# Performance work log

Hardware: AMD Instinct MI355X
Metric: run time of the kernel (lower is better)

The kernel has to match this reference:

```python
import jax, jax.numpy as jnp
import numpy as np

N_NODES = 50000
N_EDGES = 600000
N_FEAT = 128
HIDDEN = 128
OUT_CH = 128
N_GRAPHS = 64
BN_EPS = 1e-5


def gcn_conv(x, src, dst, ew, W, b):
    """PyG GCNConv: add self-loops, symmetric deg^{-1/2} normalization with edge weights."""
    n = x.shape[0]
    h = x @ W  # [N, out]
    loop = jnp.arange(n)
    src2 = jnp.concatenate([src, loop])
    dst2 = jnp.concatenate([dst, loop])
    w2 = jnp.concatenate([ew, jnp.ones((n,), x.dtype)])
    deg = jax.ops.segment_sum(w2, dst2, num_segments=n)
    dinv = jnp.where(deg > 0, jax.lax.rsqrt(deg), 0.0)
    norm = dinv[src2] * w2 * dinv[dst2]  # [E+N]
    out = jax.ops.segment_sum(h[src2] * norm[:, None], dst2, num_segments=n)
    return out + b


def setup_inputs() -> dict:
    key = jax.random.key(0)
    ks = jax.random.split(key, 12)
    x = jax.random.normal(ks[0], (N_NODES, N_FEAT), jnp.float32)
    edge_index = jax.random.randint(ks[1], (2, N_EDGES), 0, N_NODES, dtype=jnp.int64)
    batch = jnp.sort(jax.random.randint(ks[2], (N_NODES,), 0, N_GRAPHS, dtype=jnp.int64))
    edge_attr = jax.random.uniform(ks[3], (N_EDGES,), jnp.float32)
    s1 = 1.0 / np.sqrt(N_FEAT)
    s2 = 1.0 / np.sqrt(HIDDEN)
    s3 = 1.0 / np.sqrt(OUT_CH)
    s4 = 1.0 / np.sqrt(OUT_CH // 2)
    return {
        "x": x, "edge_index": edge_index, "batch": batch, "edge_attr": edge_attr,
        "W1": jax.random.uniform(ks[4], (N_FEAT, HIDDEN), jnp.float32, -s1, s1),
        "b1": jnp.zeros((HIDDEN,), jnp.float32),
        "W2": jax.random.uniform(ks[5], (HIDDEN, OUT_CH), jnp.float32, -s2, s2),
        "b2": jnp.zeros((OUT_CH,), jnp.float32),
        "fc1_W": jax.random.uniform(ks[6], (OUT_CH, OUT_CH // 2), jnp.float32, -s3, s3),
        "fc1_b": jax.random.uniform(ks[7], (OUT_CH // 2,), jnp.float32, -s3, s3),
        "bn_gamma": jnp.ones((OUT_CH // 2,), jnp.float32),
        "bn_beta": jnp.zeros((OUT_CH // 2,), jnp.float32),
        "fc3_W": jax.random.uniform(ks[8], (OUT_CH // 2, 1), jnp.float32, -s4, s4),
        "fc3_b": jax.random.uniform(ks[9], (1,), jnp.float32, -s4, s4),
    }


def reference(x, edge_index, batch, edge_attr, W1, b1, W2, b2,
              fc1_W, fc1_b, bn_gamma, bn_beta, fc3_W, fc3_b):
    src, dst = edge_index[0], edge_index[1]
    h = jax.nn.relu(gcn_conv(x, src, dst, edge_attr, W1, b1))
    # dropout skipped (deterministic eval: mode=False)
    h = jax.nn.relu(gcn_conv(h, src, dst, edge_attr, W2, b2))
    # global_mean_pool over batch segment ids
    sums = jax.ops.segment_sum(h, batch, num_segments=N_GRAPHS)  # [G, out]
    cnt = jax.ops.segment_sum(jnp.ones_like(batch, jnp.float32), batch, num_segments=N_GRAPHS)
    g = sums / jnp.maximum(cnt, 1.0)[:, None]
    z = jax.nn.relu(g @ fc1_W + fc1_b)
    # BatchNorm1d with batch statistics (training-mode math, biased var)
    mean = jnp.mean(z, axis=0)
    var = jnp.mean((z - mean) ** 2, axis=0)
    z = bn_gamma * (z - mean) * jax.lax.rsqrt(var + BN_EPS) + bn_beta
    return z @ fc3_W + fc3_b  # [G, 1]
```

## Files before the change

### kernel.cpp

```cpp
#include <hip/hip_runtime.h>

#define NNODES 50000
#define NEDGES 600000
#define NGRAPHS 64
#define BN_EPS 1e-5f
#define NB1 ((NNODES + 255) / 256)
#define PPG 16
#define GEMM_BLOCKS ((NNODES + 127) / 128)
#define NOWN 8
#define RANGE 6250
#define SEG 16
#define SEGI4 (NEDGES / SEG / 4)
#define HIST_BLOCKS (NOWN * SEG)


__device__ __forceinline__ void gemm_tile(const float* __restrict__ A,
        const float* __restrict__ W, float* __restrict__ C, int block) {
    __shared__ float a_lds[16][132];
    __shared__ float w_lds[16][192];
    const int tid = threadIdx.x;
    const int row0 = block * 128;
    const int tx = tid & 15;
    const int ty = tid >> 4;
    float acc[4][8];
#pragma unroll
    for (int i = 0; i < 4; ++i)
#pragma unroll
        for (int j = 0; j < 8; ++j) acc[i][j] = 0.f;

    for (int kc = 0; kc < 128; kc += 16) {
        {
            int r = tid >> 2;
            int k4 = (tid & 3) << 2;
            int grow = row0 + r;
            float4 v = make_float4(0.f, 0.f, 0.f, 0.f);
            if (grow < NNODES) v = *(const float4*)(A + (size_t)grow * 128 + kc + k4);
            a_lds[k4 + 0][r] = v.x; a_lds[k4 + 1][r] = v.y;
            a_lds[k4 + 2][r] = v.z; a_lds[k4 + 3][r] = v.w;
        }
        {
            int kk = tid >> 5;
            int c4 = tid & 31;
            float4 v = *(const float4*)(W + (size_t)(kc + kk) * 128 + c4 * 4);
            int sw = 12 * (c4 >> 1) + ((c4 & 1) << 2);
            *(float4*)&w_lds[kk][sw] = v;
        }
        __syncthreads();
#pragma unroll
        for (int k = 0; k < 16; ++k) {
            float a[4], b[8];
            *(float4*)&a[0] = *(const float4*)&a_lds[k][ty * 4];
            *(float4*)&b[0] = *(const float4*)&w_lds[k][tx * 12];
            *(float4*)&b[4] = *(const float4*)&w_lds[k][tx * 12 + 4];
#pragma unroll
            for (int i = 0; i < 4; ++i)
#pragma unroll
                for (int j = 0; j < 8; ++j)
                    acc[i][j] = fmaf(a[i], b[j], acc[i][j]);
        }
        __syncthreads();
    }
#pragma unroll
    for (int i = 0; i < 4; ++i) {
        int grow = row0 + ty * 4 + i;
        if (grow < NNODES) {
            float4 v0 = make_float4(acc[i][0], acc[i][1], acc[i][2], acc[i][3]);
            float4 v1 = make_float4(acc[i][4], acc[i][5], acc[i][6], acc[i][7]);
            *(float4*)(C + (size_t)grow * 128 + tx * 8) = v0;
            *(float4*)(C + (size_t)grow * 128 + tx * 8 + 4) = v1;
        }
    }
}

__global__ __launch_bounds__(512) void k_gemm1_hist(const float* __restrict__ A,
        const float* __restrict__ W, float* __restrict__ C,
        const int* __restrict__ dst, int* __restrict__ cnt_seg) {
    if (blockIdx.x >= GEMM_BLOCKS) {
        __shared__ int lh[RANGE];
        int t = threadIdx.x;
        int hb = blockIdx.x - GEMM_BLOCKS;
        int own = hb & (NOWN - 1);
        int seg = hb >> 3;
        int lo = own * RANGE;
        for (int i = t; i < RANGE; i += 512) lh[i] = 0;
        __syncthreads();
        const int4* d4 = (const int4*)dst;
        int q1 = (seg + 1) * SEGI4;
        for (int q = seg * SEGI4 + t; q < q1; q += 512) {
            int4 v = d4[q];
            unsigned a0 = (unsigned)(v.x - lo);
            unsigned a1 = (unsigned)(v.y - lo);
            unsigned a2 = (unsigned)(v.z - lo);
            unsigned a3 = (unsigned)(v.w - lo);
            if (a0 < (unsigned)RANGE) atomicAdd(&lh[a0], 1);
            if (a1 < (unsigned)RANGE) atomicAdd(&lh[a1], 1);
            if (a2 < (unsigned)RANGE) atomicAdd(&lh[a2], 1);
            if (a3 < (unsigned)RANGE) atomicAdd(&lh[a3], 1);
        }
        __syncthreads();
        for (int i = t; i < RANGE; i += 512) cnt_seg[(size_t)seg * NNODES + lo + i] = lh[i];
        return;
    }
    gemm_tile(A, W, C, blockIdx.x);
}

__global__ __launch_bounds__(512) void k_gemm(const float* __restrict__ A,
        const float* __restrict__ W, float* __restrict__ C) {
    gemm_tile(A, W, C, blockIdx.x);
}


__global__ __launch_bounds__(256) void k_scan1(const int* __restrict__ cnt_seg,
        int* __restrict__ excl, int* __restrict__ bsum) {
    __shared__ int sh[256];
    int b = blockIdx.x, t = threadIdx.x;
    int idx = b * 256 + t;
    int v = 0;
    if (idx < NNODES) {
#pragma unroll
        for (int s = 0; s < SEG; ++s) v += cnt_seg[(size_t)s * NNODES + idx];
    }
    sh[t] = v;
    __syncthreads();
#pragma unroll
    for (int off = 1; off < 256; off <<= 1) {
        int x = (t >= off) ? sh[t - off] : 0;
        __syncthreads();
        sh[t] += x;
        __syncthreads();
    }
    if (idx < NNODES) excl[idx] = sh[t] - v;
    if (t == 255) bsum[b] = sh[255];
}

__global__ __launch_bounds__(256) void k_scan2(int* __restrict__ bsum) {
    __shared__ int sh[256];
    int t = threadIdx.x;
    int v = (t < NB1) ? bsum[t] : 0;
    sh[t] = v;
    __syncthreads();
#pragma unroll
    for (int off = 1; off < 256; off <<= 1) {
        int x = (t >= off) ? sh[t - off] : 0;
        __syncthreads();
        sh[t] += x;
        __syncthreads();
    }
    if (t < NB1) bsum[t] = sh[t] - v;
}

__global__ __launch_bounds__(256) void k_scan3base(const int* __restrict__ excl,
        const int* __restrict__ bsum, const int* __restrict__ cnt_seg,
        int* __restrict__ row_start, int* __restrict__ base) {
    int b = blockIdx.x, t = threadIdx.x;
    int idx = b * 256 + t;
    if (idx >= NNODES) return;
    int rs = excl[idx] + bsum[b];
    row_start[idx] = rs;
    if (idx == 0) row_start[NNODES] = NEDGES;
    int run = rs;
#pragma unroll
    for (int s = 0; s < SEG; ++s) {
        int c = cnt_seg[(size_t)s * NNODES + idx];
        base[(size_t)s * NNODES + idx] = run;
        run += c;
    }
}


__global__ __launch_bounds__(512) void k_place_seg(const int* __restrict__ dst,
        const int* __restrict__ src, const float* __restrict__ ew,
        const int* __restrict__ base, int2* __restrict__ csr_pk) {
    __shared__ int lh[RANGE];
    int t = threadIdx.x;
    int own = blockIdx.x & (NOWN - 1);
    int seg = blockIdx.x >> 3;
    int lo = own * RANGE;
    for (int i = t; i < RANGE; i += 512) lh[i] = 0;
    __syncthreads();
    const int4* d4 = (const int4*)dst;
    const int4* s4 = (const int4*)src;
    const float4* w4 = (const float4*)ew;
    int q1 = (seg + 1) * SEGI4;
    for (int q = seg * SEGI4 + t; q < q1; q += 512) {
        int4 v = d4[q];
        int4 s = s4[q];
        float4 w = w4[q];
        unsigned a0 = (unsigned)(v.x - lo);
        unsigned a1 = (unsigned)(v.y - lo);
        unsigned a2 = (unsigned)(v.z - lo);
        unsigned a3 = (unsigned)(v.w - lo);
        if (a0 < (unsigned)RANGE) {
            int tk = atomicAdd(&lh[a0], 1);
            csr_pk[base[(size_t)seg * NNODES + v.x] + tk] = make_int2(s.x, __float_as_int(w.x));
        }
        if (a1 < (unsigned)RANGE) {
            int tk = atomicAdd(&lh[a1], 1);
            csr_pk[base[(size_t)seg * NNODES + v.y] + tk] = make_int2(s.y, __float_as_int(w.y));
        }
        if (a2 < (unsigned)RANGE) {
            int tk = atomicAdd(&lh[a2], 1);
            csr_pk[base[(size_t)seg * NNODES + v.z] + tk] = make_int2(s.z, __float_as_int(w.z));
        }
        if (a3 < (unsigned)RANGE) {
            int tk = atomicAdd(&lh[a3], 1);
            csr_pk[base[(size_t)seg * NNODES + v.w] + tk] = make_int2(s.w, __float_as_int(w.w));
        }
    }
}

__global__ __launch_bounds__(256) void k_deg(const int* __restrict__ row_start,
        const int2* __restrict__ csr_pk, float* __restrict__ dinv) {
    int i = blockIdx.x * 256 + threadIdx.x;
    if (i >= NNODES) return;
    int e0 = row_start[i], e1 = row_start[i + 1];
    float deg = 1.f;
    for (int e = e0; e < e1; ++e) deg += __int_as_float(csr_pk[e].y);
    dinv[i] = rsqrtf(deg);
}


__global__ __launch_bounds__(256) void k_aggregate(const float* __restrict__ h,
        const float* __restrict__ dinv, const int* __restrict__ row_start,
        const int2* __restrict__ csr_pk, const float* __restrict__ bias,
        float* __restrict__ out) {
    int gtid = blockIdx.x * 256 + threadIdx.x;
    int i = gtid >> 5;
    int lane = (gtid & 31) << 2;
    if (i >= NNODES) return;
    float di = dinv[i];
    float sw = di * di;
    float4 hv = *(const float4*)(h + (size_t)i * 128 + lane);
    float ax = sw * hv.x, ay = sw * hv.y, az = sw * hv.z, aw = sw * hv.w;
    int e = row_start[i];
    int e1 = row_start[i + 1];
    for (; e + 3 < e1; e += 4) {
        int2 p0 = csr_pk[e], p1 = csr_pk[e + 1], p2 = csr_pk[e + 2], p3 = csr_pk[e + 3];
        float d0 = dinv[p0.x], d1 = dinv[p1.x], d2 = dinv[p2.x], d3 = dinv[p3.x];
        float4 v0 = *(const float4*)(h + (size_t)p0.x * 128 + lane);
        float4 v1 = *(const float4*)(h + (size_t)p1.x * 128 + lane);
        float4 v2 = *(const float4*)(h + (size_t)p2.x * 128 + lane);
        float4 v3 = *(const float4*)(h + (size_t)p3.x * 128 + lane);
        float w0 = d0 * __int_as_float(p0.y) * di;
        float w1 = d1 * __int_as_float(p1.y) * di;
        float w2 = d2 * __int_as_float(p2.y) * di;
        float w3 = d3 * __int_as_float(p3.y) * di;
        ax = fmaf(w0, v0.x, ax); ay = fmaf(w0, v0.y, ay);
        az = fmaf(w0, v0.z, az); aw = fmaf(w0, v0.w, aw);
        ax = fmaf(w1, v1.x, ax); ay = fmaf(w1, v1.y, ay);
        az = fmaf(w1, v1.z, az); aw = fmaf(w1, v1.w, aw);
        ax = fmaf(w2, v2.x, ax); ay = fmaf(w2, v2.y, ay);
        az = fmaf(w2, v2.z, az); aw = fmaf(w2, v2.w, aw);
        ax = fmaf(w3, v3.x, ax); ay = fmaf(w3, v3.y, ay);
        az = fmaf(w3, v3.z, az); aw = fmaf(w3, v3.w, aw);
    }
    for (; e < e1; ++e) {
        int2 p0 = csr_pk[e];
        float w0 = dinv[p0.x] * __int_as_float(p0.y) * di;
        float4 v0 = *(const float4*)(h + (size_t)p0.x * 128 + lane);
        ax = fmaf(w0, v0.x, ax); ay = fmaf(w0, v0.y, ay);
        az = fmaf(w0, v0.z, az); aw = fmaf(w0, v0.w, aw);
    }
    float4 b = *(const float4*)(bias + lane);
    float4 o;
    o.x = fmaxf(ax + b.x, 0.f);
    o.y = fmaxf(ay + b.y, 0.f);
    o.z = fmaxf(az + b.z, 0.f);
    o.w = fmaxf(aw + b.w, 0.f);
    *(float4*)(out + (size_t)i * 128 + lane) = o;
}


__global__ __launch_bounds__(256) void k_pool1(const float* __restrict__ h2,
        const int* __restrict__ batch, float* __restrict__ part) {
    __shared__ float sh[256];
    int g = blockIdx.x / PPG;
    int p = blockIdx.x % PPG;
    int t = threadIdx.x;
    int lo = 0, hi = NNODES;
    while (lo < hi) { int mid = (lo + hi) >> 1; if (batch[mid] < g) lo = mid + 1; else hi = mid; }
    int b0 = lo;
    lo = 0; hi = NNODES;
    int g1 = g + 1;
    while (lo < hi) { int mid = (lo + hi) >> 1; if (batch[mid] < g1) lo = mid + 1; else hi = mid; }
    int b1 = lo;

    int c = t & 127, q = t >> 7;
    float acc = 0.f;
    for (int r = b0 + p * 2 + q; r < b1; r += PPG * 2) acc += h2[(size_t)r * 128 + c];
    sh[t] = acc;
    __syncthreads();
    if (t < 128) part[((size_t)g * PPG + p) * 128 + t] = sh[t] + sh[t + 128];
}

__global__ __launch_bounds__(128) void k_pool2(const float* __restrict__ part,
        const int* __restrict__ batch, float* __restrict__ gmean) {
    int g = blockIdx.x;
    int t = threadIdx.x;
    int lo = 0, hi = NNODES;
    while (lo < hi) { int mid = (lo + hi) >> 1; if (batch[mid] < g) lo = mid + 1; else hi = mid; }
    int b0 = lo;
    lo = 0; hi = NNODES;
    int g1 = g + 1;
    while (lo < hi) { int mid = (lo + hi) >> 1; if (batch[mid] < g1) lo = mid + 1; else hi = mid; }
    int b1 = lo;
    float s = 0.f;
#pragma unroll
    for (int p = 0; p < PPG; ++p) s += part[((size_t)g * PPG + p) * 128 + t];
    float n = (float)(b1 - b0);
    gmean[g * 128 + t] = s / fmaxf(n, 1.f);
}


__global__ __launch_bounds__(256) void k_head(const float* __restrict__ gmean,
        const float* __restrict__ fc1W, const float* __restrict__ fc1b,
        const float* __restrict__ gamma, const float* __restrict__ beta,
        const float* __restrict__ fc3W, const float* __restrict__ fc3b,
        float* __restrict__ out) {
    __shared__ float g[64][129];
    __shared__ float w[128][64];
    __shared__ float z[64][65];
    __shared__ float mu[64], isd[64];
    int t = threadIdx.x;
#pragma unroll
    for (int p = 0; p < 8; ++p) {
        int idx4 = p * 256 + t;
        int gg = idx4 >> 5;
        int c4 = (idx4 & 31) << 2;
        float4 v = *(const float4*)(gmean + gg * 128 + c4);
        *(float4*)&g[gg][c4] = v;
    }
#pragma unroll
    for (int p = 0; p < 8; ++p) {
        int idx4 = p * 256 + t;
        float4 v = *(const float4*)(fc1W + idx4 * 4);
        ((float4*)&w[0][0])[idx4] = v;
    }
    __syncthreads();
    int r = t >> 2;
    int c0 = (t & 3) * 16;
    float acc[16];
#pragma unroll
    for (int j = 0; j < 16; ++j) acc[j] = 0.f;
    for (int k = 0; k < 128; ++k) {
        float gv = g[r][k];
#pragma unroll
        for (int j = 0; j < 16; ++j) acc[j] = fmaf(gv, w[k][c0 + j], acc[j]);
    }
#pragma unroll
    for (int j = 0; j < 16; ++j)
        z[r][c0 + j] = fmaxf(acc[j] + fc1b[c0 + j], 0.f);
    __syncthreads();
    if (t < 64) {
        float m = 0.f;
        for (int rr = 0; rr < 64; ++rr) m += z[rr][t];
        m *= (1.f / 64.f);
        float v = 0.f;
        for (int rr = 0; rr < 64; ++rr) { float d = z[rr][t] - m; v = fmaf(d, d, v); }
        v *= (1.f / 64.f);
        mu[t] = m;
        isd[t] = rsqrtf(v + BN_EPS);
    }
    __syncthreads();
    if (t < 64) {
        float a2 = fc3b[0];
        for (int cc = 0; cc < 64; ++cc) {
            float zn = fmaf(gamma[cc] * (z[t][cc] - mu[cc]), isd[cc], beta[cc]);
            a2 = fmaf(zn, fc3W[cc], a2);
        }
        out[t] = a2;
    }
}


extern "C" void kernel_launch(void* const* d_in, const int* in_sizes, int n_in,
                              void* d_out, int out_size, void* d_ws, size_t ws_size,
                              hipStream_t stream) {
    const float* x    = (const float*)d_in[0];
    const int*   ei   = (const int*)d_in[1];
    const int*   batch= (const int*)d_in[2];
    const float* ew   = (const float*)d_in[3];
    const float* W1   = (const float*)d_in[4];
    const float* b1   = (const float*)d_in[5];
    const float* W2   = (const float*)d_in[6];
    const float* b2   = (const float*)d_in[7];
    const float* fc1W = (const float*)d_in[8];
    const float* fc1b = (const float*)d_in[9];
    const float* gam  = (const float*)d_in[10];
    const float* bet  = (const float*)d_in[11];
    const float* fc3W = (const float*)d_in[12];
    const float* fc3b = (const float*)d_in[13];
    float* out = (float*)d_out;
    const int* srcp = ei;
    const int* dstp = ei + NEDGES;

    char* wsb = (char*)d_ws;
    size_t off = 0;
    auto alloc = [&](size_t bytes) {
        void* p = wsb + off;
        off = (off + bytes + 255) & ~(size_t)255;
        return p;
    };
    float* dinv      = (float*)alloc(NNODES * 4);
    int*   row_start = (int*)alloc((NNODES + 1) * 4);
    int*   cnt_seg   = (int*)alloc((size_t)SEG * NNODES * 4);
    int*   base      = (int*)alloc((size_t)SEG * NNODES * 4);
    int*   excl      = (int*)alloc(NNODES * 4);
    int*   bsum      = (int*)alloc(NB1 * 4);
    int2*  csr_pk    = (int2*)alloc((size_t)NEDGES * 8);
    float* hbuf      = (float*)alloc((size_t)NNODES * 128 * 4);
    float* abuf      = (float*)alloc((size_t)NNODES * 128 * 4);
    float* part      = (float*)alloc((size_t)NGRAPHS * PPG * 128 * 4);
    float* gmean     = (float*)alloc(NGRAPHS * 128 * 4);
    (void)ws_size; (void)in_sizes; (void)n_in; (void)out_size;

    k_gemm1_hist<<<GEMM_BLOCKS + HIST_BLOCKS, 512, 0, stream>>>(x, W1, hbuf, dstp, cnt_seg);
    k_scan1<<<NB1, 256, 0, stream>>>(cnt_seg, excl, bsum);
    k_scan2<<<1, 256, 0, stream>>>(bsum);
    k_scan3base<<<NB1, 256, 0, stream>>>(excl, bsum, cnt_seg, row_start, base);
    k_place_seg<<<HIST_BLOCKS, 512, 0, stream>>>(dstp, srcp, ew, base, csr_pk);
    k_deg<<<NB1, 256, 0, stream>>>(row_start, csr_pk, dinv);

    k_aggregate<<<(NNODES * 32 + 255) / 256, 256, 0, stream>>>(hbuf, dinv, row_start,
                                                               csr_pk, b1, abuf);
    k_gemm<<<GEMM_BLOCKS, 512, 0, stream>>>(abuf, W2, hbuf);
    k_aggregate<<<(NNODES * 32 + 255) / 256, 256, 0, stream>>>(hbuf, dinv, row_start,
                                                               csr_pk, b2, abuf);
    k_pool1<<<NGRAPHS * PPG, 256, 0, stream>>>(abuf, batch, part);
    k_pool2<<<NGRAPHS, 128, 0, stream>>>(part, batch, gmean);
    k_head<<<1, 256, 0, stream>>>(gmean, fc1W, fc1b, gam, bet, fc3W, fc3b, out);
}
```

Baseline: 230.3 us.

## Fuse first aggregation with second GEMM and fold scan2 into scan3

Merges the layer-1 aggregation (with bias and ReLU) and the layer-2 weight multiply into one kernel. Each node's aggregated row goes to LDS and is multiplied by W2, which is read straight from global memory. This drops the standalone GEMM launch and one full write and read of the N×128 intermediate. It also removes the single-block scan2 kernel: each scan3 block now reduces the preceding block sums itself. The trade-off is a naive per-row GEMM with no register tiling and heavy W2 traffic from L2, which may be slower than the tiled GEMM it replaces.

```diff
diff --git a/kernel.cpp b/kernel.cpp
--- a/kernel.cpp
+++ b/kernel.cpp
@@ -104,11 +104,6 @@
     gemm_tile(A, W, C, blockIdx.x);
 }
 
-__global__ __launch_bounds__(512) void k_gemm(const float* __restrict__ A,
-        const float* __restrict__ W, float* __restrict__ C) {
-    gemm_tile(A, W, C, blockIdx.x);
-}
-
 
 __global__ __launch_bounds__(256) void k_scan1(const int* __restrict__ cnt_seg,
         int* __restrict__ excl, int* __restrict__ bsum) {
@@ -133,29 +128,22 @@
     if (t == 255) bsum[b] = sh[255];
 }
 
-__global__ __launch_bounds__(256) void k_scan2(int* __restrict__ bsum) {
-    __shared__ int sh[256];
-    int t = threadIdx.x;
-    int v = (t < NB1) ? bsum[t] : 0;
-    sh[t] = v;
-    __syncthreads();
-#pragma unroll
-    for (int off = 1; off < 256; off <<= 1) {
-        int x = (t >= off) ? sh[t - off] : 0;
-        __syncthreads();
-        sh[t] += x;
-        __syncthreads();
-    }
-    if (t < NB1) bsum[t] = sh[t] - v;
-}
-
 __global__ __launch_bounds__(256) void k_scan3base(const int* __restrict__ excl,
         const int* __restrict__ bsum, const int* __restrict__ cnt_seg,
         int* __restrict__ row_start, int* __restrict__ base) {
+    __shared__ int sh[256];
     int b = blockIdx.x, t = threadIdx.x;
+    sh[t] = (t < b) ? bsum[t] : 0;
+    __syncthreads();
+#pragma unroll
+    for (int off = 128; off > 0; off >>= 1) {
+        if (t < off) sh[t] += sh[t + off];
+        __syncthreads();
+    }
+    int prefix = sh[0];
     int idx = b * 256 + t;
     if (idx >= NNODES) return;
-    int rs = excl[idx] + bsum[b];
+    int rs = excl[idx] + prefix;
     row_start[idx] = rs;
     if (idx == 0) row_start[NNODES] = NEDGES;
     int run = rs;
@@ -217,6 +205,77 @@
     float deg = 1.f;
     for (int e = e0; e < e1; ++e) deg += __int_as_float(csr_pk[e].y);
     dinv[i] = rsqrtf(deg);
+}
+
+
+__global__ __launch_bounds__(256) void k_agg_gemm(const float* __restrict__ h,
+        const float* __restrict__ dinv, const int* __restrict__ row_start,
+        const int2* __restrict__ csr_pk, const float* __restrict__ bias,
+        const float* __restrict__ W2, float* __restrict__ out) {
+    __shared__ float rowbuf[8][128];
+    int gtid = blockIdx.x * 256 + threadIdx.x;
+    int i = gtid >> 5;
+    int n = (threadIdx.x >> 5);
+    int lane = (gtid & 31) << 2;
+    float di = dinv[i];
+    float sw = di * di;
+    float4 hv = *(const float4*)(h + (size_t)i * 128 + lane);
+    float ax = sw * hv.x, ay = sw * hv.y, az = sw * hv.z, aw = sw * hv.w;
+    int e = row_start[i];
+    int e1 = row_start[i + 1];
+    for (; e + 3 < e1; e += 4) {
+        int2 p0 = csr_pk[e], p1 = csr_pk[e + 1], p2 = csr_pk[e + 2], p3 = csr_pk[e + 3];
+        float d0 = dinv[p0.x], d1 = dinv[p1.x], d2 = dinv[p2.x], d3 = dinv[p3.x];
+        float4 v0 = *(const float4*)(h + (size_t)p0.x * 128 + lane);
+        float4 v1 = *(const float4*)(h + (size_t)p1.x * 128 + lane);
+        float4 v2 = *(const float4*)(h + (size_t)p2.x * 128 + lane);
+        float4 v3 = *(const float4*)(h + (size_t)p3.x * 128 + lane);
+        float w0 = d0 * __int_as_float(p0.y) * di;
+        float w1 = d1 * __int_as_float(p1.y) * di;
+        float w2 = d2 * __int_as_float(p2.y) * di;
+        float w3 = d3 * __int_as_float(p3.y) * di;
+        ax = fmaf(w0, v0.x, ax); ay = fmaf(w0, v0.y, ay);
+        az = fmaf(w0, v0.z, az); aw = fmaf(w0, v0.w, aw);
+        ax = fmaf(w1, v1.x, ax); ay = fmaf(w1, v1.y, ay);
+        az = fmaf(w1, v1.z, az); aw = fmaf(w1, v1.w, aw);
+        ax = fmaf(w2, v2.x, ax); ay = fmaf(w2, v2.y, ay);
+        az = fmaf(w2, v2.z, az); aw = fmaf(w2, v2.w, aw);
+        ax = fmaf(w3, v3.x, ax); ay = fmaf(w3, v3.y, ay);
+        az = fmaf(w3, v3.z, az); aw = fmaf(w3, v3.w, aw);
+    }
+    for (; e < e1; ++e) {
+        int2 p0 = csr_pk[e];
+        float w0 = dinv[p0.x] * __int_as_float(p0.y) * di;
+        float4 v0 = *(const float4*)(h + (size_t)p0.x * 128 + lane);
+        ax = fmaf(w0, v0.x, ax); ay = fmaf(w0, v0.y, ay);
+        az = fmaf(w0, v0.z, az); aw = fmaf(w0, v0.w, aw);
+    }
+    float4 b = *(const float4*)(bias + lane);
+    rowbuf[n][lane + 0] = fmaxf(ax + b.x, 0.f);
+    rowbuf[n][lane + 1] = fmaxf(ay + b.y, 0.f);
+    rowbuf[n][lane + 2] = fmaxf(az + b.z, 0.f);
+    rowbuf[n][lane + 3] = fmaxf(aw + b.w, 0.f);
+    __syncthreads();
+    const float4* w4 = (const float4*)W2;
+    int l = (gtid & 31);
+    float acc0 = 0.f, acc1 = 0.f, acc2 = 0.f, acc3 = 0.f;
+    for (int k = 0; k < 128; k += 4) {
+        float4 r = *(const float4*)&rowbuf[n][k];
+        float4 wa = w4[(k + 0) * 32 + l];
+        float4 wb = w4[(k + 1) * 32 + l];
+        float4 wc = w4[(k + 2) * 32 + l];
+        float4 wd = w4[(k + 3) * 32 + l];
+        acc0 = fmaf(r.x, wa.x, acc0); acc1 = fmaf(r.x, wa.y, acc1);
+        acc2 = fmaf(r.x, wa.z, acc2); acc3 = fmaf(r.x, wa.w, acc3);
+        acc0 = fmaf(r.y, wb.x, acc0); acc1 = fmaf(r.y, wb.y, acc1);
+        acc2 = fmaf(r.y, wb.z, acc2); acc3 = fmaf(r.y, wb.w, acc3);
+        acc0 = fmaf(r.z, wc.x, acc0); acc1 = fmaf(r.z, wc.y, acc1);
+        acc2 = fmaf(r.z, wc.z, acc2); acc3 = fmaf(r.z, wc.w, acc3);
+        acc0 = fmaf(r.w, wd.x, acc0); acc1 = fmaf(r.w, wd.y, acc1);
+        acc2 = fmaf(r.w, wd.z, acc2); acc3 = fmaf(r.w, wd.w, acc3);
+    }
+    float4 o = make_float4(acc0, acc1, acc2, acc3);
+    *(float4*)(out + (size_t)i * 128 + lane) = o;
 }
 
 
@@ -416,17 +475,15 @@
 
     k_gemm1_hist<<<GEMM_BLOCKS + HIST_BLOCKS, 512, 0, stream>>>(x, W1, hbuf, dstp, cnt_seg);
     k_scan1<<<NB1, 256, 0, stream>>>(cnt_seg, excl, bsum);
-    k_scan2<<<1, 256, 0, stream>>>(bsum);
     k_scan3base<<<NB1, 256, 0, stream>>>(excl, bsum, cnt_seg, row_start, base);
     k_place_seg<<<HIST_BLOCKS, 512, 0, stream>>>(dstp, srcp, ew, base, csr_pk);
     k_deg<<<NB1, 256, 0, stream>>>(row_start, csr_pk, dinv);
 
-    k_aggregate<<<(NNODES * 32 + 255) / 256, 256, 0, stream>>>(hbuf, dinv, row_start,
-                                                               csr_pk, b1, abuf);
-    k_gemm<<<GEMM_BLOCKS, 512, 0, stream>>>(abuf, W2, hbuf);
-    k_aggregate<<<(NNODES * 32 + 255) / 256, 256, 0, stream>>>(hbuf, dinv, row_start,
-                                                               csr_pk, b2, abuf);
-    k_pool1<<<NGRAPHS * PPG, 256, 0, stream>>>(abuf, batch, part);
+    k_agg_gemm<<<(NNODES * 32) / 256, 256, 0, stream>>>(hbuf, dinv, row_start,
+                                                        csr_pk, b1, W2, abuf);
+    k_aggregate<<<(NNODES * 32 + 255) / 256, 256, 0, stream>>>(abuf, dinv, row_start,
+                                                               csr_pk, b2, hbuf);
+    k_pool1<<<NGRAPHS * PPG, 256, 0, stream>>>(hbuf, batch, part);
     k_pool2<<<NGRAPHS, 128, 0, stream>>>(part, batch, gmean);
     k_head<<<1, 256, 0, stream>>>(gmean, fc1W, fc1b, gam, bet, fc3W, fc3b, out);
 }
```

Result: slower. 272.4 us (+18.3%).
